# Kernel optimization log

Measured on AMD Instinct MI355X. Metric: run time of the kernel, lower is better.

The kernel has to match this reference:

```python
import jax, jax.numpy as jnp
import numpy as np

N = 100000          # num nodes
E = 3200000         # num edges (avg degree 32)
G = 64              # num graphs in batch
F_IN = 2            # num_node_features
H = 16              # hidden_size
NUM_LAYERS = 2


def sage_conv(x, src, dst, W_l, b_l, W_r):
    # PyG SAGEConv (mean aggr): out = lin_l(mean_{j in N(i)} x_j) + lin_r(x_i)
    msg = x[src]                                                  # [E, F] gather
    agg = jax.ops.segment_sum(msg, dst, num_segments=N)          # [N, F] scatter-add
    deg = jax.ops.segment_sum(jnp.ones((src.shape[0],), x.dtype), dst, num_segments=N)
    mean = agg / jnp.maximum(deg, 1.0)[:, None]
    return mean @ W_l + b_l + x @ W_r


def setup_inputs() -> dict:
    key = jax.random.key(0)
    ks = jax.random.split(key, 10)
    x = jax.random.normal(ks[0], (N, F_IN), dtype=jnp.float32)
    edge_index = jax.random.randint(ks[1], (2, E), 0, N, dtype=jnp.int64)
    batch = jnp.sort(jax.random.randint(ks[2], (N,), 0, G, dtype=jnp.int64))
    s1 = 1.0 / np.sqrt(F_IN)
    s2 = 1.0 / np.sqrt(H)
    return {
        "x": x,
        "edge_index": edge_index,
        "batch": batch,
        "W1_l": jax.random.uniform(ks[3], (F_IN, H), jnp.float32, -s1, s1),
        "b1_l": jnp.zeros((H,), jnp.float32),
        "W1_r": jax.random.uniform(ks[4], (F_IN, H), jnp.float32, -s1, s1),
        "W2_l": jax.random.uniform(ks[5], (H, H), jnp.float32, -s2, s2),
        "b2_l": jnp.zeros((H,), jnp.float32),
        "W2_r": jax.random.uniform(ks[6], (H, H), jnp.float32, -s2, s2),
        "W_end": jax.random.uniform(ks[7], (H, 1), jnp.float32, -s2, s2),
        "b_end": jnp.zeros((1,), jnp.float32),
    }


def reference(x, edge_index, batch, W1_l, b1_l, W1_r, W2_l, b2_l, W2_r, W_end, b_end):
    src, dst = edge_index[0], edge_index[1]
    h = sage_conv(x, src, dst, W1_l, b1_l, W1_r)                 # conv1
    for _ in range(NUM_LAYERS - 1):
        h = jax.nn.relu(h)
        h = sage_conv(h, src, dst, W2_l, b2_l, W2_r)             # conv2
    h = jax.nn.relu(h)
    # dropout is identity in eval mode
    h = h @ W_end + b_end                                         # [N, 1]
    # global mean pool over graphs
    summed = jax.ops.segment_sum(h, batch, num_segments=G)       # [G, 1]
    counts = jax.ops.segment_sum(jnp.ones((N,), h.dtype), batch, num_segments=G)
    pooled = summed / jnp.maximum(counts, 1.0)[:, None]
    return jax.nn.sigmoid(pooled)                                 # [G, 1]
```

## Files before the change

kernel.cpp:

```cpp
#include <hip/hip_runtime.h>
#include <math.h>

#define NN 100000
#define NE 3200000
#define NG 64
#define HID 16
#define EPB 8192
#define NBLKE ((NE + EPB - 1) / EPB)
#define NBUCK ((NN + 255) / 256)
#define LMAX 10240

typedef unsigned int uint;


__device__ inline uint bf16pair(float a, float b) {
    uint ua = __float_as_uint(a), ub = __float_as_uint(b);
    ua = (ua + 0x7fffu + ((ua >> 16) & 1u)) >> 16;
    ub = (ub + 0x7fffu + ((ub >> 16) & 1u)) >> 16;
    return ua | (ub << 16);
}

__global__ __launch_bounds__(512) void k_bhist(const int* __restrict__ dst,
                                               int* __restrict__ blockCnt) {
    __shared__ int h[NBUCK];
    int t = threadIdx.x;
    for (int i = t; i < NBUCK; i += 512) h[i] = 0;
    __syncthreads();
    int base = blockIdx.x * EPB;
    int n4 = (min(base + EPB, NE) - base) >> 2;
    const int4* d4 = (const int4*)(dst + base);
    for (int i = t; i < n4; i += 512) {
        int4 v = d4[i];
        atomicAdd(&h[v.x >> 8], 1);
        atomicAdd(&h[v.y >> 8], 1);
        atomicAdd(&h[v.z >> 8], 1);
        atomicAdd(&h[v.w >> 8], 1);
    }
    __syncthreads();
    for (int i = t; i < NBUCK; i += 512)
        blockCnt[blockIdx.x * NBUCK + i] = h[i];
}

__global__ __launch_bounds__(512) void k_bucketscan(int* __restrict__ blockCnt,
                                                    int* __restrict__ bucketTot) {
    __shared__ int a[512];
    int t = threadIdx.x, b = blockIdx.x;
    a[t] = (t < NBLKE) ? blockCnt[t * NBUCK + b] : 0;
    __syncthreads();
    for (int off = 1; off < 512; off <<= 1) {
        int x = a[t] + ((t >= off) ? a[t - off] : 0);
        __syncthreads();
        a[t] = x;
        __syncthreads();
    }
    if (t < NBLKE) blockCnt[t * NBUCK + b] = (t ? a[t - 1] : 0);
    if (t == 0) bucketTot[b] = a[511];
}

__global__ __launch_bounds__(512) void k_basescan(const int* __restrict__ bucketTot,
                                                  int* __restrict__ bucketBase,
                                                  int* __restrict__ offs) {
    __shared__ int a[512];
    int t = threadIdx.x;
    a[t] = (t < NBUCK) ? bucketTot[t] : 0;
    __syncthreads();
    for (int off = 1; off < 512; off <<= 1) {
        int x = a[t] + ((t >= off) ? a[t - off] : 0);
        __syncthreads();
        a[t] = x;
        __syncthreads();
    }
    if (t < NBUCK) bucketBase[t] = (t ? a[t - 1] : 0);
    if (t == 0) { bucketBase[NBUCK] = a[511]; offs[NN] = a[511]; }
}

__global__ __launch_bounds__(512) void k_bscatter(const int* __restrict__ src,
                                                  const int* __restrict__ dst,
                                                  const int* __restrict__ blockCnt,
                                                  const int* __restrict__ bucketBase,
                                                  int* __restrict__ pairs) {
    __shared__ int cur[NBUCK];
    int t = threadIdx.x;
    for (int i = t; i < NBUCK; i += 512)
        cur[i] = blockCnt[blockIdx.x * NBUCK + i] + bucketBase[i];
    __syncthreads();
    int base = blockIdx.x * EPB;
    int n4 = (min(base + EPB, NE) - base) >> 2;
    const int4* d4 = (const int4*)(dst + base);
    const int4* s4 = (const int4*)(src + base);
    for (int i = t; i < n4; i += 512) {
        int4 dv = d4[i];
        int4 sv = s4[i];
        int p0 = atomicAdd(&cur[dv.x >> 8], 1);
        pairs[p0] = (sv.x << 8) | (dv.x & 255);
        int p1 = atomicAdd(&cur[dv.y >> 8], 1);
        pairs[p1] = (sv.y << 8) | (dv.y & 255);
        int p2 = atomicAdd(&cur[dv.z >> 8], 1);
        pairs[p2] = (sv.z << 8) | (dv.z & 255);
        int p3 = atomicAdd(&cur[dv.w >> 8], 1);
        pairs[p3] = (sv.w << 8) | (dv.w & 255);
    }
}

__global__ __launch_bounds__(512) void k_fill2c1(
    const int* __restrict__ bucketBase, const int* __restrict__ pairs,
    const float* __restrict__ x,
    const float* __restrict__ W1l, const float* __restrict__ b1l,
    const float* __restrict__ W1r,
    int* __restrict__ offs, int* __restrict__ csr, uint* __restrict__ h1u) {
    __shared__ int a[256];
    __shared__ int lcur[256];
    __shared__ int lss[LMAX];
    int t = threadIdx.x, b = blockIdx.x;
    int pb = bucketBase[b], pe = bucketBase[b + 1];
    if (t < 256) a[t] = 0;
    __syncthreads();
    for (int e = pb + t; e < pe; e += 512)
        atomicAdd(&a[pairs[e] & 255], 1);
    __syncthreads();
    for (int off = 1; off < 256; off <<= 1) {
        int v = 0;
        if (t < 256) v = a[t] + ((t >= off) ? a[t - off] : 0);
        __syncthreads();
        if (t < 256) a[t] = v;
        __syncthreads();
    }
    if (t < 256) lcur[t] = t ? a[t - 1] : 0;
    __syncthreads();
    for (int e = pb + t; e < pe; e += 512) {
        int v = pairs[e];
        int s = v >> 8, dl = v & 255;
        int lpos = atomicAdd(&lcur[dl], 1);
        csr[pb + lpos] = s;
        if (lpos < LMAX) lss[lpos] = s;
    }
    __syncthreads();
    if (t < 256) {
        int node = b * 256 + t;
        if (node < NN) {
            int excl = t ? a[t - 1] : 0;
            int cntn = a[t] - excl;
            offs[node] = pb + excl;
            float s0 = 0.f, s1 = 0.f;
            for (int k = 0; k < cntn; ++k) {
                int idx = excl + k;
                int s = (idx < LMAX) ? lss[idx] : csr[pb + idx];
                float2 xv = *(const float2*)(x + 2 * s);
                s0 += xv.x; s1 += xv.y;
            }
            float inv = 1.0f / fmaxf((float)cntn, 1.0f);
            float m0 = s0 * inv, m1 = s1 * inv;
            float x0 = x[2 * node], x1 = x[2 * node + 1];
            float o[16];
#pragma unroll
            for (int h = 0; h < 16; ++h)
                o[h] = fmaxf(m0 * W1l[h] + m1 * W1l[16 + h] + b1l[h]
                           + x0 * W1r[h] + x1 * W1r[16 + h], 0.f);
            uint4 o0, o1;
            o0.x = bf16pair(o[0], o[1]);   o0.y = bf16pair(o[2], o[3]);
            o0.z = bf16pair(o[4], o[5]);   o0.w = bf16pair(o[6], o[7]);
            o1.x = bf16pair(o[8], o[9]);   o1.y = bf16pair(o[10], o[11]);
            o1.z = bf16pair(o[12], o[13]); o1.w = bf16pair(o[14], o[15]);
            uint4* d4 = (uint4*)(h1u + (size_t)node * 8);
            d4[0] = o0; d4[1] = o1;
        }
    }
}

__global__ __launch_bounds__(256) void k_conv2pool(
    const int* __restrict__ offs, const int* __restrict__ csr,
    const uint* __restrict__ h1u,
    const float* __restrict__ W2l, const float* __restrict__ b2l,
    const float* __restrict__ W2r, const float* __restrict__ Wend,
    const float* __restrict__ bend, const int* __restrict__ batch,
    float* __restrict__ gsum, float* __restrict__ gcnt) {
    __shared__ float sWl[256], sWr[256], sB[HID], sWe[HID];
    __shared__ float sm[32][17], shr[32][17];
    __shared__ float ls[NG], lc[NG];
    int t = threadIdx.x;
    sWl[t] = W2l[t];
    sWr[t] = W2r[t];
    if (t < HID) { sB[t] = b2l[t]; sWe[t] = Wend[t]; }
    if (t < NG) { ls[t] = 0.f; lc[t] = 0.f; }

    int g = t >> 3;
    int l8 = t & 7;
    int gbase = (t & 63) & 56;
    int i = blockIdx.x * 32 + g;
    int beg = offs[i], end = offs[i + 1];
    float acc0 = 0.f, acc1 = 0.f;
    int kb = beg;
    for (; kb + 8 <= end; kb += 8) {
        int sv = csr[kb + l8];
#pragma unroll
        for (int j = 0; j < 8; ++j) {
            int s = __shfl(sv, gbase + j, 64);
            uint u = h1u[(size_t)s * 8 + l8];
            acc0 += __uint_as_float(u << 16);
            acc1 += __uint_as_float(u & 0xffff0000u);
        }
    }
    if (kb < end) {
        int idx = kb + l8;
        int sv = (idx < end) ? csr[idx] : 0;
        int nb = end - kb;
        for (int j = 0; j < nb; ++j) {
            int s = __shfl(sv, gbase + j, 64);
            uint u = h1u[(size_t)s * 8 + l8];
            acc0 += __uint_as_float(u << 16);
            acc1 += __uint_as_float(u & 0xffff0000u);
        }
    }
    float inv = 1.0f / fmaxf((float)(end - beg), 1.0f);
    uint us = h1u[(size_t)i * 8 + l8];
    sm[g][2 * l8]      = acc0 * inv;
    sm[g][2 * l8 + 1]  = acc1 * inv;
    shr[g][2 * l8]     = __uint_as_float(us << 16);
    shr[g][2 * l8 + 1] = __uint_as_float(us & 0xffff0000u);
    __syncthreads();

    int h0 = l8, h1 = l8 + 8;
    float a0 = sB[h0], a1 = sB[h1];
#pragma unroll
    for (int ff = 0; ff < HID; ++ff) {
        float m = sm[g][ff], r = shr[g][ff];
        a0 += m * sWl[ff * HID + h0] + r * sWr[ff * HID + h0];
        a1 += m * sWl[ff * HID + h1] + r * sWr[ff * HID + h1];
    }
    float y = fmaxf(a0, 0.f) * sWe[h0] + fmaxf(a1, 0.f) * sWe[h1];
    y += __shfl_xor(y, 1, 64);
    y += __shfl_xor(y, 2, 64);
    y += __shfl_xor(y, 4, 64);
    if (l8 == 0) {
        int bg = batch[i];
        atomicAdd(&ls[bg], y + bend[0]);
        atomicAdd(&lc[bg], 1.0f);
    }
    __syncthreads();
    if (t < NG && lc[t] != 0.0f) {
        unsafeAtomicAdd(&gsum[t], ls[t]);
        unsafeAtomicAdd(&gcnt[t], lc[t]);
    }
}

__global__ void k_final(const float* __restrict__ gsum, const float* __restrict__ gcnt,
                        float* __restrict__ out) {
    int g = threadIdx.x;
    if (g < NG) {
        float p = gsum[g] / fmaxf(gcnt[g], 1.0f);
        out[g] = 1.0f / (1.0f + expf(-p));
    }
}

extern "C" void kernel_launch(void* const* d_in, const int* in_sizes, int n_in,
                              void* d_out, int out_size, void* d_ws, size_t ws_size,
                              hipStream_t stream) {
    const float* x    = (const float*)d_in[0];
    const int*   ei   = (const int*)d_in[1];
    const int*   batch= (const int*)d_in[2];
    const float* W1l  = (const float*)d_in[3];
    const float* b1l  = (const float*)d_in[4];
    const float* W1r  = (const float*)d_in[5];
    const float* W2l  = (const float*)d_in[6];
    const float* b2l  = (const float*)d_in[7];
    const float* W2r  = (const float*)d_in[8];
    const float* Wend = (const float*)d_in[9];
    const float* bend = (const float*)d_in[10];

    const int* src = ei;
    const int* dst = ei + NE;

    float* gsum      = (float*)d_ws;
    float* gcnt      = (float*)d_ws + NG;
    int*   blockCnt  = (int*)d_ws + 2 * NG;
    int*   bucketTot = blockCnt + (size_t)NBLKE * NBUCK;
    int*   bucketBase= bucketTot + NBUCK;
    int*   offs      = bucketBase + NBUCK + 1;
    size_t po        = (size_t)(offs - (int*)d_ws) + NN + 1;
    po               = (po + 3) & ~(size_t)3;
    int*   pairs     = (int*)d_ws + po;
    int*   csr       = pairs + NE;
    uint*  h1u       = (uint*)(csr + NE);

    hipMemsetAsync(d_ws, 0, 2 * NG * sizeof(float), stream);

    k_bhist     <<<NBLKE, 512, 0, stream>>>(dst, blockCnt);
    k_bucketscan<<<NBUCK, 512, 0, stream>>>(blockCnt, bucketTot);
    k_basescan  <<<1, 512, 0, stream>>>(bucketTot, bucketBase, offs);
    k_bscatter  <<<NBLKE, 512, 0, stream>>>(src, dst, blockCnt, bucketBase, pairs);
    k_fill2c1   <<<NBUCK, 512, 0, stream>>>(bucketBase, pairs, x, W1l, b1l, W1r,
                                            offs, csr, h1u);
    k_conv2pool <<<NN / 32, 256, 0, stream>>>(offs, csr, h1u, W2l, b2l, W2r,
                                              Wend, bend, batch, gsum, gcnt);
    k_final     <<<1, 64, 0, stream>>>(gsum, gcnt, (float*)d_out);
}
```

Measured before the change: 122.8 us.

## Transpose block-count layout, fold memset into scan, batch neighbor gathers

Stores per-block bucket counts bucket-major so the per-bucket scan reads contiguous memory, at the cost of strided writes in the histogram and scatter kernels. Moves zeroing of the pooling accumulators into the single-block base scan kernel, removing a separate memset launch. In the second convolution, issues 16 neighbor gathers into a register buffer before accumulating, so more loads are in flight at once, at the cost of extra registers.

```diff
diff --git a/kernel.cpp b/kernel.cpp
--- a/kernel.cpp
+++ b/kernel.cpp
@@ -38,14 +38,14 @@
     }
     __syncthreads();
     for (int i = t; i < NBUCK; i += 512)
-        blockCnt[blockIdx.x * NBUCK + i] = h[i];
+        blockCnt[i * NBLKE + blockIdx.x] = h[i];
 }
 
 __global__ __launch_bounds__(512) void k_bucketscan(int* __restrict__ blockCnt,
                                                     int* __restrict__ bucketTot) {
     __shared__ int a[512];
     int t = threadIdx.x, b = blockIdx.x;
-    a[t] = (t < NBLKE) ? blockCnt[t * NBUCK + b] : 0;
+    a[t] = (t < NBLKE) ? blockCnt[b * NBLKE + t] : 0;
     __syncthreads();
     for (int off = 1; off < 512; off <<= 1) {
         int x = a[t] + ((t >= off) ? a[t - off] : 0);
@@ -53,15 +53,18 @@
         a[t] = x;
         __syncthreads();
     }
-    if (t < NBLKE) blockCnt[t * NBUCK + b] = (t ? a[t - 1] : 0);
+    if (t < NBLKE) blockCnt[b * NBLKE + t] = (t ? a[t - 1] : 0);
     if (t == 0) bucketTot[b] = a[511];
 }
 
 __global__ __launch_bounds__(512) void k_basescan(const int* __restrict__ bucketTot,
                                                   int* __restrict__ bucketBase,
-                                                  int* __restrict__ offs) {
+                                                  int* __restrict__ offs,
+                                                  float* __restrict__ gsum,
+                                                  float* __restrict__ gcnt) {
     __shared__ int a[512];
     int t = threadIdx.x;
+    if (t < NG) { gsum[t] = 0.f; gcnt[t] = 0.f; }
     a[t] = (t < NBUCK) ? bucketTot[t] : 0;
     __syncthreads();
     for (int off = 1; off < 512; off <<= 1) {
@@ -82,7 +85,7 @@
     __shared__ int cur[NBUCK];
     int t = threadIdx.x;
     for (int i = t; i < NBUCK; i += 512)
-        cur[i] = blockCnt[blockIdx.x * NBUCK + i] + bucketBase[i];
+        cur[i] = blockCnt[i * NBLKE + blockIdx.x] + bucketBase[i];
     __syncthreads();
     int base = blockIdx.x * EPB;
     int n4 = (min(base + EPB, NE) - base) >> 2;
@@ -190,14 +193,37 @@
     int beg = offs[i], end = offs[i + 1];
     float acc0 = 0.f, acc1 = 0.f;
     int kb = beg;
+    uint ubuf[16];
+    for (; kb + 16 <= end; kb += 16) {
+        int sv0 = csr[kb + l8];
+        int sv1 = csr[kb + 8 + l8];
+#pragma unroll
+        for (int j = 0; j < 8; ++j) {
+            int s = __shfl(sv0, gbase + j, 64);
+            ubuf[j] = h1u[(size_t)s * 8 + l8];
+        }
+#pragma unroll
+        for (int j = 0; j < 8; ++j) {
+            int s = __shfl(sv1, gbase + j, 64);
+            ubuf[8 + j] = h1u[(size_t)s * 8 + l8];
+        }
+#pragma unroll
+        for (int j = 0; j < 16; ++j) {
+            acc0 += __uint_as_float(ubuf[j] << 16);
+            acc1 += __uint_as_float(ubuf[j] & 0xffff0000u);
+        }
+    }
     for (; kb + 8 <= end; kb += 8) {
         int sv = csr[kb + l8];
 #pragma unroll
         for (int j = 0; j < 8; ++j) {
             int s = __shfl(sv, gbase + j, 64);
-            uint u = h1u[(size_t)s * 8 + l8];
-            acc0 += __uint_as_float(u << 16);
-            acc1 += __uint_as_float(u & 0xffff0000u);
+            ubuf[j] = h1u[(size_t)s * 8 + l8];
+        }
+#pragma unroll
+        for (int j = 0; j < 8; ++j) {
+            acc0 += __uint_as_float(ubuf[j] << 16);
+            acc1 += __uint_as_float(ubuf[j] & 0xffff0000u);
         }
     }
     if (kb < end) {
@@ -282,11 +308,9 @@
     int*   csr       = pairs + NE;
     uint*  h1u       = (uint*)(csr + NE);
 
-    hipMemsetAsync(d_ws, 0, 2 * NG * sizeof(float), stream);
-
     k_bhist     <<<NBLKE, 512, 0, stream>>>(dst, blockCnt);
     k_bucketscan<<<NBUCK, 512, 0, stream>>>(blockCnt, bucketTot);
-    k_basescan  <<<1, 512, 0, stream>>>(bucketTot, bucketBase, offs);
+    k_basescan  <<<1, 512, 0, stream>>>(bucketTot, bucketBase, offs, gsum, gcnt);
     k_bscatter  <<<NBLKE, 512, 0, stream>>>(src, dst, blockCnt, bucketBase, pairs);
     k_fill2c1   <<<NBUCK, 512, 0, stream>>>(bucketBase, pairs, x, W1l, b1l, W1r,
                                             offs, csr, h1u);
```

New measurement: 117.2 us. -4.5%, faster.
